# Optimization experiments

Measured on AMD Instinct MI355X. Metric: run time of the kernel, lower is better.

## Reference

```python
import jax, jax.numpy as jnp
import numpy as np

B, T, E, A = 4, 4096, 1024, 1024

def setup_inputs() -> dict:
    key = jax.random.key(0)
    k1, k2, k3, k4 = jax.random.split(key, 4)
    scale = 1.0 / np.sqrt(E)  # ~ nn.Linear default init scale
    return {
        "embedded": jax.random.normal(k1, (B, T, E), dtype=jnp.float32),
        "Wq": jax.random.uniform(k2, (A, E), jnp.float32, -scale, scale),
        "Wk": jax.random.uniform(k3, (A, E), jnp.float32, -scale, scale),
        "Wv": jax.random.uniform(k4, (A, E), jnp.float32, -scale, scale),
    }

def reference(embedded, Wq, Wk, Wv):
    # QKV projections (nn.Linear without bias: x @ W.T)
    q = jnp.einsum('bte,ae->bta', embedded, Wq)
    k = jnp.einsum('bte,ae->bta', embedded, Wk)
    v = jnp.einsum('bte,ae->bta', embedded, Wv)
    A_dim = q.shape[-1]
    # scaled scores [B, T, T]
    scores = jnp.einsum('bqa,bka->bqk', q, k) / jnp.sqrt(jnp.float32(A_dim))
    # causal mask (lower triangular allowed)
    Tq = scores.shape[-1]
    causal = jnp.tril(jnp.ones((Tq, Tq), dtype=bool))
    scores = jnp.where(causal, scores, -jnp.inf)
    probs = jax.nn.softmax(scores, axis=-1)
    out = jnp.einsum('bqk,bka->bqa', probs, v)
    return jnp.round(out, 4)
```

## Files before the change

### kernel.cpp

```cpp
#include <hip/hip_runtime.h>
#include <hip/hip_bf16.h>

using bf16 = __hip_bfloat16;

typedef __attribute__((ext_vector_type(4))) float f32x4;
typedef __attribute__((ext_vector_type(8))) short short8;

typedef const void __attribute__((address_space(1)))* gas1_t;
typedef void __attribute__((address_space(3)))* las3_t;
#define GLDS(gp, lp) __builtin_amdgcn_global_load_lds((gas1_t)(gp), (las3_t)(lp), 16, 0, 0)

__device__ inline short f2bfbits(float f) {
  union { bf16 h; short s; } u;
  u.h = __float2bfloat16(f);
  return u.s;
}
__device__ inline float bf2f(short u) {
  unsigned x = ((unsigned)(unsigned short)u) << 16;
  float f; __builtin_memcpy(&f, &x, 4); return f;
}

__device__ inline void store_out(float* C, size_t idx, float v) { C[idx] = v; }
__device__ inline void store_out(bf16* C, size_t idx, float v) { C[idx] = __float2bfloat16(v); }

template<typename TOUT, int MODE>
__global__ __launch_bounds__(512, 2) void gemm256(
    const short* __restrict__ A, int lda, size_t sAz,
    const short* __restrict__ B, int ldb, size_t sBz,
    TOUT* __restrict__ C, int ldc, size_t sCz,
    int K, float scale)
{
  int bx, by;
  if constexpr (MODE == 1) {
    const int i = blockIdx.x;
    by = (int)((__builtin_sqrtf(8.f * (float)i + 1.f) - 1.f) * 0.5f);
    if (((by * (by + 1)) >> 1) > i) by--;
    else if ((((by + 1) * (by + 2)) >> 1) <= i) by++;
    bx = i - ((by * (by + 1)) >> 1);
  } else {
    bx = blockIdx.x; by = blockIdx.y;
  }
  const int z = blockIdx.z;
  const int tri_by = (by * (by + 1)) >> 1;

  A += (size_t)z * sAz;
  B += (size_t)z * sBz;
  C += (size_t)z * sCz;

  int Klen = K;
  if (MODE == 2) Klen = min(K, (by + 1) * 256);
  const int NT = Klen >> 5;

  __shared__ short As[3][256 * 32];
  __shared__ short Bs[3][256 * 32];

  const int t = threadIdx.x;
  const int lane = t & 63;
  const int wave = t >> 6;
  const int wm = wave >> 2;
  const int wn = wave & 3;
  const int fr = lane & 15, kh = lane >> 4;
  const int koff = ((kh ^ ((fr >> 1) & 3)) << 3);

  int srow[2], scol[2];
  #pragma unroll
  for (int j = 0; j < 2; j++) {
    int e = j * 512 + t;
    srow[j] = e >> 2;
    scol[j] = (((e & 3) ^ ((e >> 3) & 3)) << 3);
  }

  f32x4 acc[8][4];
  #pragma unroll
  for (int i = 0; i < 8; i++)
    #pragma unroll
    for (int j = 0; j < 4; j++) acc[i][j] = (f32x4){0.f, 0.f, 0.f, 0.f};

  auto STAGE_A = [&](int kt) {
    const int buf = kt % 3, k0 = kt * 32;
    #pragma unroll
    for (int j = 0; j < 2; j++) {
      const short* pa;
      if constexpr (MODE == 2)
        pa = A + (size_t)(tri_by + (k0 >> 8)) * 65536 + (size_t)srow[j] * 256 + (k0 & 255) + scol[j];
      else
        pa = A + (size_t)(by * 256 + srow[j]) * lda + k0 + scol[j];
      GLDS(pa, (char*)&As[buf][0] + j * 8192 + wave * 1024);
    }
  };
  auto STAGE_B = [&](int kt) {
    const int buf = kt % 3, k0 = kt * 32;
    #pragma unroll
    for (int j = 0; j < 2; j++) {
      const short* pb = B + (size_t)(bx * 256 + srow[j]) * ldb + k0 + scol[j];
      GLDS(pb, (char*)&Bs[buf][0] + j * 8192 + wave * 1024);
    }
  };

  STAGE_A(0); STAGE_B(0);
  STAGE_A(1); STAGE_B(1);
  asm volatile("s_waitcnt vmcnt(4)\ns_barrier" ::: "memory");

  const int arow = wm * 128 + fr;
  const int brow = wn * 64 + fr;

  for (int kt = 0; kt < NT; kt++) {
    const short* as = &As[kt % 3][0];
    const short* bs = &Bs[kt % 3][0];
    short8 af[4], bfr[4];

    #pragma unroll
    for (int n = 0; n < 4; n++) bfr[n] = *(const short8*)&bs[(brow + n * 16) * 32 + koff];
    #pragma unroll
    for (int m = 0; m < 4; m++) af[m] = *(const short8*)&as[(arow + m * 16) * 32 + koff];
    if (kt + 2 < NT) STAGE_A(kt + 2);
    __builtin_amdgcn_s_barrier();
    asm volatile("s_waitcnt lgkmcnt(0)" ::: "memory");
    __builtin_amdgcn_sched_barrier(0);
    __builtin_amdgcn_s_setprio(1);
    #pragma unroll
    for (int m = 0; m < 4; m++)
      #pragma unroll
      for (int n = 0; n < 4; n++)
        acc[m][n] = __builtin_amdgcn_mfma_f32_16x16x32_bf16(af[m], bfr[n], acc[m][n], 0, 0, 0);
    __builtin_amdgcn_s_setprio(0);
    __builtin_amdgcn_sched_barrier(0);

    #pragma unroll
    for (int m = 0; m < 4; m++) af[m] = *(const short8*)&as[(arow + (m + 4) * 16) * 32 + koff];
    if (kt + 2 < NT) STAGE_B(kt + 2);
    __builtin_amdgcn_s_barrier();
    asm volatile("s_waitcnt lgkmcnt(0)" ::: "memory");
    __builtin_amdgcn_sched_barrier(0);
    __builtin_amdgcn_s_setprio(1);
    #pragma unroll
    for (int m = 0; m < 4; m++)
      #pragma unroll
      for (int n = 0; n < 4; n++)
        acc[m + 4][n] = __builtin_amdgcn_mfma_f32_16x16x32_bf16(af[m], bfr[n], acc[m + 4][n], 0, 0, 0);
    __builtin_amdgcn_s_setprio(0);
    __builtin_amdgcn_sched_barrier(0);

    if (kt + 2 < NT)      asm volatile("s_waitcnt vmcnt(4)\ns_barrier" ::: "memory");
    else if (kt + 1 < NT) asm volatile("s_waitcnt vmcnt(0)\ns_barrier" ::: "memory");
  }

  #pragma unroll
  for (int m = 0; m < 8; m++)
    #pragma unroll
    for (int n = 0; n < 4; n++) {
      int col_l = wn * 64 + n * 16 + fr;
      #pragma unroll
      for (int r = 0; r < 4; r++) {
        int row_l = wm * 128 + m * 16 + kh * 4 + r;
        if constexpr (MODE == 1)
          store_out(C, (size_t)(tri_by + bx) * 65536 + (size_t)row_l * 256 + col_l,
                    acc[m][n][r] * scale);
        else
          store_out(C, (size_t)(by * 256 + row_l) * ldc + bx * 256 + col_l,
                    acc[m][n][r] * scale);
      }
    }
}

__global__ __launch_bounds__(256) void cvt_bf16(
    const float* __restrict__ in, bf16* __restrict__ out, int n, float scale)
{
  for (int i = (blockIdx.x * 256 + threadIdx.x) * 8; i < n; i += gridDim.x * 2048) {
    f32x4 v0 = *(const f32x4*)&in[i];
    f32x4 v1 = *(const f32x4*)&in[i + 4];
    short8 o = { f2bfbits(v0[0] * scale), f2bfbits(v0[1] * scale),
                 f2bfbits(v0[2] * scale), f2bfbits(v0[3] * scale),
                 f2bfbits(v1[0] * scale), f2bfbits(v1[1] * scale),
                 f2bfbits(v1[2] * scale), f2bfbits(v1[3] * scale) };
    *(short8*)&out[i] = o;
  }
}

__global__ __launch_bounds__(256) void softmax_causal_packed(short* SP, int T)
{
  __shared__ float rowv[4096];
  __shared__ float red[4];
  const int r = blockIdx.x;
  const int z = blockIdx.y;
  const int rb = r >> 8, rl = r & 255;
  const size_t tri = (size_t)((rb * (rb + 1)) >> 1);
  short* base = SP + (size_t)z * 136 * 65536;
  const int L = r + 1;
  const int kend = (rb + 1) * 256;
  const int t = threadIdx.x;

  float lmax = -3.0e38f;
  for (int i = t * 8; i < kend; i += 2048) {
    short8 s = *(const short8*)(base + (tri + (i >> 8)) * 65536 + (size_t)rl * 256 + (i & 255));
    #pragma unroll
    for (int j = 0; j < 8; j++) {
      float v = bf2f(s[j]);
      rowv[i + j] = v;
      if (i + j < L) lmax = fmaxf(lmax, v);
    }
  }
  #pragma unroll
  for (int o = 32; o > 0; o >>= 1) lmax = fmaxf(lmax, __shfl_down(lmax, o));
  if ((t & 63) == 0) red[t >> 6] = lmax;
  __syncthreads();
  const float m = fmaxf(fmaxf(red[0], red[1]), fmaxf(red[2], red[3]));
  __syncthreads();

  float lsum = 0.f;
  for (int i = t; i < kend; i += 256) {
    float e = (i < L) ? __expf(rowv[i] - m) : 0.f;
    rowv[i] = e;
    lsum += e;
  }
  #pragma unroll
  for (int o = 32; o > 0; o >>= 1) lsum += __shfl_down(lsum, o);
  if ((t & 63) == 0) red[t >> 6] = lsum;
  __syncthreads();
  const float inv = 1.f / (red[0] + red[1] + red[2] + red[3]);

  for (int i = t * 8; i < kend; i += 2048) {
    short8 o;
    #pragma unroll
    for (int j = 0; j < 8; j++) o[j] = f2bfbits(rowv[i + j] * inv);
    *(short8*)(base + (tri + (i >> 8)) * 65536 + (size_t)rl * 256 + (i & 255)) = o;
  }
}

extern "C" void kernel_launch(void* const* d_in, const int* in_sizes, int n_in,
                              void* d_out, int out_size, void* d_ws, size_t ws_size,
                              hipStream_t stream) {
  (void)in_sizes; (void)n_in; (void)out_size; (void)ws_size;
  const float* X  = (const float*)d_in[0];
  const float* Wq = (const float*)d_in[1];
  const float* Wk = (const float*)d_in[2];
  const float* Wv = (const float*)d_in[3];
  float* Out = (float*)d_out;

  const int Bn = 4, T = 4096, E = 1024, Ad = 1024;
  const int M = Bn * T;

  char* ws = (char*)d_ws;
  short* QKb = (short*)ws;
  short* Vt  = (short*)(ws + 67108864);
  short* Xb  = (short*)(ws + 100663296);
  short* Wqk = (short*)(ws + 134217728);
  short* Wvb = (short*)(ws + 138412032);
  short* SP  = (short*)(ws + 100663296);

  dim3 blk(256), blk5(512);
  const float qscale = 0.03125f;
  const size_t SPz = (size_t)136 * 65536;

  cvt_bf16<<<dim3(8192), blk, 0, stream>>>(X, (bf16*)Xb, M * E, 1.0f);
  cvt_bf16<<<dim3(512),  blk, 0, stream>>>(Wq, (bf16*)Wqk, Ad * E, qscale);
  cvt_bf16<<<dim3(512),  blk, 0, stream>>>(Wk, (bf16*)(Wqk + (size_t)Ad * E), Ad * E, 1.0f);
  cvt_bf16<<<dim3(512),  blk, 0, stream>>>(Wv, (bf16*)Wvb, Ad * E, 1.0f);

  gemm256<bf16, 0><<<dim3(2048 / 256, M / 256), blk5, 0, stream>>>(
      Xb, E, 0, Wqk, E, 0, (bf16*)QKb, 2048, 0, E, 1.0f);
  gemm256<bf16, 0><<<dim3(M / 256, Ad / 256), blk5, 0, stream>>>(
      Wvb, E, 0, Xb, E, 0, (bf16*)Vt, M, 0, E, 1.0f);

  gemm256<bf16, 1><<<dim3(136, 1, Bn), blk5, 0, stream>>>(
      QKb, 2048, (size_t)T * 2048,
      QKb + 1024, 2048, (size_t)T * 2048,
      (bf16*)SP, 256, SPz, Ad, 1.0f);

  softmax_causal_packed<<<dim3(T, Bn), blk, 0, stream>>>(SP, T);

  gemm256<float, 2><<<dim3(Ad / 256, T / 256, Bn), blk5, 0, stream>>>(
      SP, 256, SPz,
      Vt, M, (size_t)T,
      Out, Ad, (size_t)T * Ad, T, 1.0f);
}
```

Baseline: 399.2 us.

## Fold Wk^T Wq into one weight matrix to skip the K projection

Uses the identity q·k = x_q (Wq^T Wk) x_k^T: it precomputes W2 = Wk^T·Wq (scaled) with a small new GEMM on transposed bf16 weights. The Q projection now multiplies by W2, and scores are computed directly against the bf16 input X, so the K projection GEMM is removed. This halves the N dimension of the projection GEMM and adds a 1024^3 weight product plus two transpose-convert kernels. The extra bf16 rounding of W2 may change numerical error.

Result: faster. 384.1 us (-3.8%).

```diff
diff --git a/kernel.cpp b/kernel.cpp
--- a/kernel.cpp
+++ b/kernel.cpp
@@ -163,6 +163,65 @@
     }
 }
 
+__global__ __launch_bounds__(256) void gemm128(
+    const short* __restrict__ A, int lda,
+    const short* __restrict__ B, int ldb,
+    bf16* __restrict__ C, int ldc, int K, float scale)
+{
+  const int bx = blockIdx.x, by = blockIdx.y;
+  __shared__ short a_lds[128 * 32];
+  __shared__ short b_lds[128 * 32];
+
+  const int t = threadIdx.x;
+  const int lane = t & 63;
+  const int wave = t >> 6;
+  const int wm = wave >> 1, wn = wave & 1;
+  const int fr = lane & 15, kh = lane >> 4;
+
+  f32x4 acc[4][4];
+  #pragma unroll
+  for (int i = 0; i < 4; i++)
+    #pragma unroll
+    for (int j = 0; j < 4; j++) acc[i][j] = (f32x4){0.f, 0.f, 0.f, 0.f};
+
+  for (int k0 = 0; k0 < K; k0 += 32) {
+    #pragma unroll
+    for (int i = 0; i < 2; i++) {
+      int e = i * 256 + t;
+      int r_ = e >> 2, c_ = (e & 3) * 8;
+      GLDS(A + (size_t)(by * 128 + r_) * lda + k0 + c_, (char*)a_lds + i * 4096 + wave * 1024);
+      GLDS(B + (size_t)(bx * 128 + r_) * ldb + k0 + c_, (char*)b_lds + i * 4096 + wave * 1024);
+    }
+    __syncthreads();
+
+    short8 af[4], bfr[4];
+    #pragma unroll
+    for (int m = 0; m < 4; m++)
+      af[m] = *(const short8*)&a_lds[(wm * 64 + m * 16 + fr) * 32 + kh * 8];
+    #pragma unroll
+    for (int n = 0; n < 4; n++)
+      bfr[n] = *(const short8*)&b_lds[(wn * 64 + n * 16 + fr) * 32 + kh * 8];
+    #pragma unroll
+    for (int m = 0; m < 4; m++)
+      #pragma unroll
+      for (int n = 0; n < 4; n++)
+        acc[m][n] = __builtin_amdgcn_mfma_f32_16x16x32_bf16(af[m], bfr[n], acc[m][n], 0, 0, 0);
+    __syncthreads();
+  }
+
+  #pragma unroll
+  for (int m = 0; m < 4; m++)
+    #pragma unroll
+    for (int n = 0; n < 4; n++) {
+      int col = bx * 128 + wn * 64 + n * 16 + fr;
+      #pragma unroll
+      for (int r = 0; r < 4; r++) {
+        int row = by * 128 + wm * 64 + m * 16 + kh * 4 + r;
+        C[(size_t)row * ldc + col] = __float2bfloat16(acc[m][n][r] * scale);
+      }
+    }
+}
+
 __global__ __launch_bounds__(256) void cvt_bf16(
     const float* __restrict__ in, bf16* __restrict__ out, int n, float scale)
 {
@@ -174,6 +233,27 @@
                  f2bfbits(v1[0] * scale), f2bfbits(v1[1] * scale),
                  f2bfbits(v1[2] * scale), f2bfbits(v1[3] * scale) };
     *(short8*)&out[i] = o;
+  }
+}
+
+__global__ __launch_bounds__(256) void cvt_t_bf16(
+    const float* __restrict__ in, bf16* __restrict__ out, int N)
+{
+  __shared__ float tile[64][65];
+  const int bx = blockIdx.x, by = blockIdx.y;
+  const int t = threadIdx.x;
+  #pragma unroll
+  for (int i = 0; i < 16; i++) {
+    int e = i * 256 + t;
+    int r = e >> 6, c = e & 63;
+    tile[r][c] = in[(size_t)(by * 64 + r) * N + bx * 64 + c];
+  }
+  __syncthreads();
+  #pragma unroll
+  for (int i = 0; i < 16; i++) {
+    int e = i * 256 + t;
+    int r = e >> 6, c = e & 63;
+    out[(size_t)(bx * 64 + r) * N + by * 64 + c] = __float2bfloat16(tile[c][r]);
   }
 }
 
@@ -241,31 +321,36 @@
   const int M = Bn * T;
 
   char* ws = (char*)d_ws;
-  short* QKb = (short*)ws;
-  short* Vt  = (short*)(ws + 67108864);
-  short* Xb  = (short*)(ws + 100663296);
-  short* Wqk = (short*)(ws + 134217728);
-  short* Wvb = (short*)(ws + 138412032);
-  short* SP  = (short*)(ws + 100663296);
+  short* Q2  = (short*)ws;
+  short* Vt  = (short*)(ws + 33554432);
+  short* Xb  = (short*)(ws + 67108864);
+  short* WqT = (short*)(ws + 100663296);
+  short* WkT = (short*)(ws + 102760448);
+  short* Wvb = (short*)(ws + 104857600);
+  short* W2T = (short*)(ws + 106954752);
+  short* SP  = (short*)(ws + 109051904);
 
   dim3 blk(256), blk5(512);
-  const float qscale = 0.03125f;
   const size_t SPz = (size_t)136 * 65536;
 
   cvt_bf16<<<dim3(8192), blk, 0, stream>>>(X, (bf16*)Xb, M * E, 1.0f);
-  cvt_bf16<<<dim3(512),  blk, 0, stream>>>(Wq, (bf16*)Wqk, Ad * E, qscale);
-  cvt_bf16<<<dim3(512),  blk, 0, stream>>>(Wk, (bf16*)(Wqk + (size_t)Ad * E), Ad * E, 1.0f);
-  cvt_bf16<<<dim3(512),  blk, 0, stream>>>(Wv, (bf16*)Wvb, Ad * E, 1.0f);
-
-  gemm256<bf16, 0><<<dim3(2048 / 256, M / 256), blk5, 0, stream>>>(
-      Xb, E, 0, Wqk, E, 0, (bf16*)QKb, 2048, 0, E, 1.0f);
+  cvt_t_bf16<<<dim3(16, 16), blk, 0, stream>>>(Wq, (bf16*)WqT, E);
+  cvt_t_bf16<<<dim3(16, 16), blk, 0, stream>>>(Wk, (bf16*)WkT, E);
+  cvt_bf16<<<dim3(512), blk, 0, stream>>>(Wv, (bf16*)Wvb, Ad * E, 1.0f);
+
+  gemm128<<<dim3(8, 8), blk, 0, stream>>>(
+      WkT, Ad, WqT, Ad, (bf16*)W2T, E, Ad, 0.03125f);
+
+  gemm256<bf16, 0><<<dim3(1024 / 256, M / 256), blk5, 0, stream>>>(
+      Xb, E, 0, W2T, E, 0, (bf16*)Q2, 1024, 0, E, 1.0f);
+
   gemm256<bf16, 0><<<dim3(M / 256, Ad / 256), blk5, 0, stream>>>(
       Wvb, E, 0, Xb, E, 0, (bf16*)Vt, M, 0, E, 1.0f);
 
   gemm256<bf16, 1><<<dim3(136, 1, Bn), blk5, 0, stream>>>(
-      QKb, 2048, (size_t)T * 2048,
-      QKb + 1024, 2048, (size_t)T * 2048,
-      (bf16*)SP, 256, SPz, Ad, 1.0f);
+      Q2, 1024, (size_t)T * 1024,
+      Xb, 1024, (size_t)T * 1024,
+      (bf16*)SP, 256, SPz, E, 1.0f);
 
   softmax_causal_packed<<<dim3(T, Bn), blk, 0, stream>>>(SP, T);
 
```
